# Kernel tuning notes

Measured on AMD Instinct MI355X. Metric: run time of the kernel, lower is better.

The kernel has to match this reference:

```python
import jax, jax.numpy as jnp
import numpy as np

N, M, D = 1024, 32, 512
EPS = 1e-6


def setup_inputs() -> dict:
    key = jax.random.key(0)
    k1, = jax.random.split(key, 1)
    dvecs = jax.random.normal(k1, (N, M, D), dtype=jnp.float32)
    w = jnp.float32(10.0)
    b = jnp.float32(-5.0)
    return {"dvecs": dvecs, "w": w, "b": b}


def reference(dvecs, w, b):
    # dvecs: (N, M, D)
    n, m, d = dvecs.shape
    centroids = dvecs.mean(axis=1)                     # (N, D) full centroids
    # leave-one-out centroid for the reference utterance's own speaker
    c_loo = (dvecs.sum(axis=1, keepdims=True) - dvecs) / (m - 1)   # (N, M, D)

    e_norm = jnp.linalg.norm(dvecs, axis=-1)           # (N, M)
    c_norm = jnp.linalg.norm(centroids, axis=-1)       # (N,)
    c_loo_norm = jnp.linalg.norm(c_loo, axis=-1)       # (N, M)

    # cosine sim against all full centroids: (N, M, N)
    cos = jnp.einsum('jmd,kd->jmk', dvecs, centroids) / (
        e_norm[:, :, None] * c_norm[None, None, :])
    # replace the own-speaker entry with leave-one-out cosine
    loo_cos = jnp.einsum('jmd,jmd->jm', dvecs, c_loo) / (e_norm * c_loo_norm)
    jidx = jnp.arange(n)
    midx = jnp.arange(m)
    cos = cos.at[jidx[:, None], midx[None, :], jidx[:, None]].set(loo_cos)

    # torch.clamp(x, 1e-6) clamps the minimum only
    cos = jnp.maximum(cos, EPS) * w + b

    # softmax embed loss: L[j,i] = -log_softmax(cos[j,i,:])[j]
    logp = jax.nn.log_softmax(cos, axis=-1)
    L = -logp[jidx[:, None], midx[None, :], jidx[:, None]]
    return L.sum()
```

## Files before the change

### kernel.cpp

```cpp
#include <hip/hip_runtime.h>
#include <hip/hip_bf16.h>

#define NSPK 1024
#define MU 32
#define DIM 512
#define DIMP (DIM + 8)
#define NROW (NSPK * MU)
#define EPS 1e-6f

typedef __attribute__((ext_vector_type(4))) float f32x4;
typedef __attribute__((ext_vector_type(2))) long i64x2;

#define GLOAD_LDS16(g, l)                                          \
  __builtin_amdgcn_global_load_lds(                                \
      (const __attribute__((address_space(1))) void*)(g),          \
      (__attribute__((address_space(3))) void*)(l), 16, 0, 0)

__global__ __launch_bounds__(256) void k_prep(
    const float* __restrict__ dvecs,
    char* __restrict__ Af8,
    char* __restrict__ Bf8,
    float* __restrict__ loo)
{
  const int j = blockIdx.x, t = threadIdx.x;
  __shared__ float sD[MU * DIMP];
  __shared__ float sS[DIM];
  __shared__ float sred[4];
  __shared__ float sS2v;
  __shared__ float sInv[MU];

  const float* base = dvecs + (size_t)j * (MU * DIM);

  float s0 = 0.f, s1 = 0.f;
  for (int m = 0; m < MU; ++m) {
    float a = base[m * DIM + t];
    float b = base[m * DIM + t + 256];
    sD[m * DIMP + t] = a;
    sD[m * DIMP + t + 256] = b;
    s0 += a; s1 += b;
  }
  sS[t] = s0; sS[t + 256] = s1;
  __syncthreads();

  float p = s0 * s0 + s1 * s1;
  for (int off = 32; off; off >>= 1) p += __shfl_down(p, off);
  if ((t & 63) == 0) sred[t >> 6] = p;
  __syncthreads();
  if (t == 0) sS2v = sred[0] + sred[1] + sred[2] + sred[3];
  __syncthreads();
  const float S2 = sS2v;

  const int g = t >> 3, l = t & 7;
  float dotS = 0.f, e2 = 0.f;
  for (int i = 0; i < DIM / 8; ++i) {
    int d = i * 8 + l;
    float ev = sD[g * DIMP + d];
    dotS += ev * sS[d];
    e2 += ev * ev;
  }
  for (int off = 4; off; off >>= 1) {
    dotS += __shfl_down(dotS, off);
    e2 += __shfl_down(e2, off);
  }
  if (l == 0) {
    float numer = dotS - e2;
    float d2 = fmaxf(S2 - 2.f * dotS + e2, 1e-30f);
    loo[j * MU + g] = numer / (sqrtf(e2) * sqrtf(d2));
    sInv[g] = 1.f / sqrtf(e2);
  }
  __syncthreads();

  for (int i = 0; i < 8; ++i) {
    int idx = i * 256 + t;
    int m = idx >> 6;
    int c = idx & 63;
    int kt = c >> 2, lk = c & 3;
    float inv = sInv[m];
    const float* src = &sD[m * DIMP + c * 8];
    int b0 = 0, b1 = 0;
    b0 = __builtin_amdgcn_cvt_pk_fp8_f32(src[0] * inv, src[1] * inv, b0, false);
    b0 = __builtin_amdgcn_cvt_pk_fp8_f32(src[2] * inv, src[3] * inv, b0, true);
    b1 = __builtin_amdgcn_cvt_pk_fp8_f32(src[4] * inv, src[5] * inv, b1, false);
    b1 = __builtin_amdgcn_cvt_pk_fp8_f32(src[6] * inv, src[7] * inv, b1, true);
    size_t byte = ((size_t)(j >> 2) << 16) + ((size_t)kt << 12) +
                  ((size_t)(j & 3) << 10) + (lk * 16 + (m & 15)) * 16 +
                  (((m >> 4) & 1) << 3);
    *(int2*)(Af8 + byte) = make_int2(b0, b1);
  }

  if (t < 64) {
    int c = t;
    int kt = c >> 2, lk = c & 3;
    float invc = 1.f / sqrtf(S2);
    const float* src = &sS[c * 8];
    int b0 = 0, b1 = 0;
    b0 = __builtin_amdgcn_cvt_pk_fp8_f32(src[0] * invc, src[1] * invc, b0, false);
    b0 = __builtin_amdgcn_cvt_pk_fp8_f32(src[2] * invc, src[3] * invc, b0, true);
    b1 = __builtin_amdgcn_cvt_pk_fp8_f32(src[4] * invc, src[5] * invc, b1, false);
    b1 = __builtin_amdgcn_cvt_pk_fp8_f32(src[6] * invc, src[7] * invc, b1, true);
    size_t byte = ((size_t)(j >> 7) << 16) + ((size_t)kt << 12) +
                  ((size_t)((j >> 5) & 3) << 10) + (lk * 16 + (j & 15)) * 16 +
                  (((j >> 4) & 1) << 3);
    *(int2*)(Bf8 + byte) = make_int2(b0, b1);
  }
}

__global__ __launch_bounds__(256, 1) void k_gemm(
    const char* __restrict__ Af8,
    const char* __restrict__ Bf8,
    const float* __restrict__ wp,
    float* __restrict__ part,
    float* __restrict__ diag)
{
  __shared__ char ldsA[4 * 4096];
  __shared__ char ldsB[4 * 4096];
  __shared__ float sPart[128][2];

  const int t = threadIdx.x;
  const int w = t >> 6, lane = t & 63;
  const int lr = lane & 15, lk = lane >> 4;
  const int wm = w >> 1, wn = w & 1;
  const int bid = blockIdx.x;
  const int xcd = bid & 7, ii = bid >> 3;
  const int rb = xcd * 32 + (ii >> 3);
  const int cb = ii & 7;

  f32x4 acc[4][4];
#pragma unroll
  for (int a = 0; a < 4; ++a)
#pragma unroll
    for (int b = 0; b < 4; ++b) acc[a][b] = (f32x4)0.f;

  const char* gA = Af8 + ((size_t)rb << 16) + t * 16;
  const char* gB = Bf8 + ((size_t)cb << 16) + t * 16;
  char* dA = &ldsA[t * 16];
  char* dB = &ldsB[t * 16];

#define STAGE(kt, bi)                                     \
  {                                                       \
    GLOAD_LDS16(gA + ((size_t)(kt) << 12), dA + ((bi) << 12)); \
    GLOAD_LDS16(gB + ((size_t)(kt) << 12), dB + ((bi) << 12)); \
  }

  i64x2 aP[2][2], bP[2][2];
  const char* lA0 = &ldsA[(wm * 2) * 1024 + lane * 16];
  const char* lB0 = &ldsB[(wn * 2) * 1024 + lane * 16];

#define DSREAD(set, bi)                                      \
  {                                                          \
    aP[set][0] = *(const i64x2*)(lA0 + ((bi) << 12));        \
    aP[set][1] = *(const i64x2*)(lA0 + ((bi) << 12) + 1024); \
    bP[set][0] = *(const i64x2*)(lB0 + ((bi) << 12));        \
    bP[set][1] = *(const i64x2*)(lB0 + ((bi) << 12) + 1024); \
  }

  STAGE(0, 0);
  STAGE(1, 1);
  STAGE(2, 2);
  asm volatile("s_waitcnt vmcnt(4)" ::: "memory");
  __builtin_amdgcn_s_barrier();
  __builtin_amdgcn_sched_barrier(0);
  DSREAD(0, 0);

#pragma unroll
  for (int kt = 0; kt < 16; ++kt) {
    if (kt <= 13) {
      asm volatile("s_waitcnt vmcnt(2)" ::: "memory");
    } else {
      asm volatile("s_waitcnt vmcnt(0)" ::: "memory");
    }
    __builtin_amdgcn_s_barrier();
    __builtin_amdgcn_sched_barrier(0);

    if (kt <= 12) STAGE(kt + 3, (kt + 3) & 3);
    if (kt < 15) DSREAD((kt + 1) & 1, (kt + 1) & 3);

    if (kt < 15) {
      asm volatile("s_waitcnt lgkmcnt(4)" ::: "memory");
    } else {
      asm volatile("s_waitcnt lgkmcnt(0)" ::: "memory");
    }
    __builtin_amdgcn_sched_barrier(0);

    {
      const int s = kt & 1;
      long av[4] = {aP[s][0].x, aP[s][0].y, aP[s][1].x, aP[s][1].y};
      long bv[4] = {bP[s][0].x, bP[s][0].y, bP[s][1].x, bP[s][1].y};
      __builtin_amdgcn_s_setprio(1);
#pragma unroll
      for (int mf = 0; mf < 4; ++mf)
#pragma unroll
        for (int nf = 0; nf < 4; ++nf)
          acc[mf][nf] = __builtin_amdgcn_mfma_f32_16x16x32_fp8_fp8(
              av[mf], bv[nf], acc[mf][nf], 0, 0, 0);
      __builtin_amdgcn_s_setprio(0);
    }
  }
#undef STAGE
#undef DSREAD

  const float W = *wp;

  if (cb == (rb >> 5)) {
#pragma unroll
    for (int sp = 0; sp < 4; ++sp) {
      const int c = rb * 4 + sp;
      if (wm == (sp >> 1) && wn == ((c >> 6) & 1)) {
        const int nfo = (c >> 4) & 3;
#pragma unroll
        for (int mh = 0; mh < 2; ++mh) {
          f32x4 dsel = acc[(sp & 1) * 2 + mh][0];
#pragma unroll
          for (int nf = 1; nf < 4; ++nf)
            if (nf == nfo) dsel = acc[(sp & 1) * 2 + mh][nf];
          if (lr == (c & 15)) {
#pragma unroll
            for (int i = 0; i < 4; ++i)
              diag[c * 32 + mh * 16 + lk * 4 + i] = dsel[i];
          }
        }
      }
    }
  }

#pragma unroll
  for (int mf = 0; mf < 4; ++mf)
#pragma unroll
    for (int i = 0; i < 4; ++i) {
      float s = 0.f;
#pragma unroll
      for (int nf = 0; nf < 4; ++nf)
        s += __expf((fmaxf(acc[mf][nf][i], EPS) - 1.f) * W);
      s += __shfl_xor(s, 1);
      s += __shfl_xor(s, 2);
      s += __shfl_xor(s, 4);
      s += __shfl_xor(s, 8);
      if (lr == 0) sPart[wm * 64 + mf * 16 + lk * 4 + i][wn] = s;
    }
  __syncthreads();
  if (t < 128)
    part[(size_t)cb * NROW + rb * 128 + t] = sPart[t][0] + sPart[t][1];
}

__global__ __launch_bounds__(256) void k_final1(
    const float* __restrict__ part, const float* __restrict__ loo,
    const float* __restrict__ diag, const float* __restrict__ wp,
    float* __restrict__ p2)
{
  const int t = threadIdx.x;
  const int r = blockIdx.x * 256 + t;
  const float W = *wp;
  float s = 0.f;
#pragma unroll
  for (int c = 0; c < 8; ++c) s += part[(size_t)c * NROW + r];
  const float lt = (fmaxf(loo[r], EPS) - 1.f) * W;
  const float dt = (fmaxf(diag[r], EPS) - 1.f) * W;
  s += __expf(lt) - __expf(dt);
  float v = logf(s) - lt;
  __shared__ float red[4];
  for (int off = 32; off; off >>= 1) v += __shfl_down(v, off);
  if ((t & 63) == 0) red[t >> 6] = v;
  __syncthreads();
  if (t == 0) p2[blockIdx.x] = red[0] + red[1] + red[2] + red[3];
}

__global__ __launch_bounds__(128) void k_final2(
    const float* __restrict__ p2, float* __restrict__ out)
{
  const int t = threadIdx.x;
  float v = p2[t];
  for (int off = 32; off; off >>= 1) v += __shfl_down(v, off);
  __shared__ float red[2];
  if ((t & 63) == 0) red[t >> 6] = v;
  __syncthreads();
  if (t == 0) out[0] = red[0] + red[1];
}

extern "C" void kernel_launch(void* const* d_in, const int* in_sizes, int n_in,
                              void* d_out, int out_size, void* d_ws, size_t ws_size,
                              hipStream_t stream) {
  const float* dvecs = (const float*)d_in[0];
  const float* wptr  = (const float*)d_in[1];
  float* out = (float*)d_out;

  char* ws = (char*)d_ws;
  char* Af8 = ws;            ws += (size_t)NROW * DIM;
  char* Bf8 = ws;            ws += (size_t)NSPK * DIM;
  float* loo  = (float*)ws;  ws += (size_t)NROW * sizeof(float);
  float* diag = (float*)ws;  ws += (size_t)NROW * sizeof(float);
  float* part = (float*)ws;  ws += (size_t)8 * NROW * sizeof(float);
  float* p2   = (float*)ws;

  k_prep<<<NSPK, 256, 0, stream>>>(dvecs, Af8, Bf8, loo);
  k_gemm<<<2048, 256, 0, stream>>>(Af8, Bf8, wptr, part, diag);
  k_final1<<<NROW / 256, 256, 0, stream>>>(part, loo, diag, wptr, p2);
  k_final2<<<1, 128, 0, stream>>>(p2, out);
}
```

Before: 66.19 us.

## Deepen GEMM LDS pipeline to six stages with two k-tiles per barrier; vectorize prep loads

The fp8 GEMM kernel's LDS ring grows from four to six buffers, and the main loop now processes two k-tiles per barrier. It issues two stage loads and two LDS reads per iteration, which halves the number of barriers and deepens the prefetch distance. Separately, the prep kernel loads its input with float4 and splits the member dimension across two thread halves before combining the partial column sums. The changes raise LDS usage and register pressure, and they drop the earlier overlap in which the next tile's LDS reads were issued before the current tile's MFMAs.

```diff
diff --git a/kernel.cpp b/kernel.cpp
--- a/kernel.cpp
+++ b/kernel.cpp
@@ -24,6 +24,7 @@
 {
   const int j = blockIdx.x, t = threadIdx.x;
   __shared__ float sD[MU * DIMP];
+  __shared__ float4 sHalf[2][128];
   __shared__ float sS[DIM];
   __shared__ float sred[4];
   __shared__ float sS2v;
@@ -31,18 +32,28 @@
 
   const float* base = dvecs + (size_t)j * (MU * DIM);
 
-  float s0 = 0.f, s1 = 0.f;
-  for (int m = 0; m < MU; ++m) {
-    float a = base[m * DIM + t];
-    float b = base[m * DIM + t + 256];
-    sD[m * DIMP + t] = a;
-    sD[m * DIMP + t + 256] = b;
-    s0 += a; s1 += b;
-  }
-  sS[t] = s0; sS[t + 256] = s1;
-  __syncthreads();
-
-  float p = s0 * s0 + s1 * s1;
+  const int h = t >> 7, c4 = t & 127;
+  {
+    const float* bp = base + h * 16 * DIM + c4 * 4;
+    float4 cs = make_float4(0.f, 0.f, 0.f, 0.f);
+#pragma unroll
+    for (int m = 0; m < 16; ++m) {
+      float4 v = *(const float4*)(bp + m * DIM);
+      *(float4*)&sD[(h * 16 + m) * DIMP + c4 * 4] = v;
+      cs.x += v.x; cs.y += v.y; cs.z += v.z; cs.w += v.w;
+    }
+    sHalf[h][c4] = cs;
+  }
+  __syncthreads();
+  if (t < 128) {
+    float4 a = sHalf[0][t], b2 = sHalf[1][t];
+    float4 s;
+    s.x = a.x + b2.x; s.y = a.y + b2.y; s.z = a.z + b2.z; s.w = a.w + b2.w;
+    *(float4*)&sS[t * 4] = s;
+  }
+  __syncthreads();
+
+  float p = sS[t] * sS[t] + sS[t + 256] * sS[t + 256];
   for (int off = 32; off; off >>= 1) p += __shfl_down(p, off);
   if ((t & 63) == 0) sred[t >> 6] = p;
   __syncthreads();
@@ -112,8 +123,8 @@
     float* __restrict__ part,
     float* __restrict__ diag)
 {
-  __shared__ char ldsA[4 * 4096];
-  __shared__ char ldsB[4 * 4096];
+  __shared__ char ldsA[6 * 4096];
+  __shared__ char ldsB[6 * 4096];
   __shared__ float sPart[128][2];
 
   const int t = threadIdx.x;
@@ -136,8 +147,8 @@
   char* dA = &ldsA[t * 16];
   char* dB = &ldsB[t * 16];
 
-#define STAGE(kt, bi)                                     \
-  {                                                       \
+#define STAGE(kt, bi)                                          \
+  {                                                            \
     GLOAD_LDS16(gA + ((size_t)(kt) << 12), dA + ((bi) << 12)); \
     GLOAD_LDS16(gB + ((size_t)(kt) << 12), dB + ((bi) << 12)); \
   }
@@ -154,50 +165,54 @@
     bP[set][1] = *(const i64x2*)(lB0 + ((bi) << 12) + 1024); \
   }
 
+#define MFMA_SET(s)                                                      \
+  {                                                                      \
+    long av[4] = {aP[s][0].x, aP[s][0].y, aP[s][1].x, aP[s][1].y};       \
+    long bv[4] = {bP[s][0].x, bP[s][0].y, bP[s][1].x, bP[s][1].y};       \
+    __builtin_amdgcn_s_setprio(1);                                       \
+    _Pragma("unroll")                                                    \
+    for (int mf = 0; mf < 4; ++mf)                                       \
+      _Pragma("unroll")                                                  \
+      for (int nf = 0; nf < 4; ++nf)                                     \
+        acc[mf][nf] = __builtin_amdgcn_mfma_f32_16x16x32_fp8_fp8(        \
+            av[mf], bv[nf], acc[mf][nf], 0, 0, 0);                       \
+    __builtin_amdgcn_s_setprio(0);                                       \
+  }
+
   STAGE(0, 0);
   STAGE(1, 1);
   STAGE(2, 2);
-  asm volatile("s_waitcnt vmcnt(4)" ::: "memory");
-  __builtin_amdgcn_s_barrier();
-  __builtin_amdgcn_sched_barrier(0);
-  DSREAD(0, 0);
-
-#pragma unroll
-  for (int kt = 0; kt < 16; ++kt) {
-    if (kt <= 13) {
-      asm volatile("s_waitcnt vmcnt(2)" ::: "memory");
+  STAGE(3, 3);
+
+#pragma unroll
+  for (int i = 0; i < 8; ++i) {
+    if (i < 7) {
+      asm volatile("s_waitcnt vmcnt(4)" ::: "memory");
     } else {
       asm volatile("s_waitcnt vmcnt(0)" ::: "memory");
     }
     __builtin_amdgcn_s_barrier();
     __builtin_amdgcn_sched_barrier(0);
 
-    if (kt <= 12) STAGE(kt + 3, (kt + 3) & 3);
-    if (kt < 15) DSREAD((kt + 1) & 1, (kt + 1) & 3);
-
-    if (kt < 15) {
-      asm volatile("s_waitcnt lgkmcnt(4)" ::: "memory");
-    } else {
-      asm volatile("s_waitcnt lgkmcnt(0)" ::: "memory");
-    }
+    if (i <= 5) {
+      STAGE(2 * i + 4, (2 * i + 4) % 6);
+      STAGE(2 * i + 5, (2 * i + 5) % 6);
+    }
+
+    DSREAD(0, (2 * i) % 6);
     __builtin_amdgcn_sched_barrier(0);
-
-    {
-      const int s = kt & 1;
-      long av[4] = {aP[s][0].x, aP[s][0].y, aP[s][1].x, aP[s][1].y};
-      long bv[4] = {bP[s][0].x, bP[s][0].y, bP[s][1].x, bP[s][1].y};
-      __builtin_amdgcn_s_setprio(1);
-#pragma unroll
-      for (int mf = 0; mf < 4; ++mf)
-#pragma unroll
-        for (int nf = 0; nf < 4; ++nf)
-          acc[mf][nf] = __builtin_amdgcn_mfma_f32_16x16x32_fp8_fp8(
-              av[mf], bv[nf], acc[mf][nf], 0, 0, 0);
-      __builtin_amdgcn_s_setprio(0);
-    }
+    DSREAD(1, (2 * i + 1) % 6);
+
+    asm volatile("s_waitcnt lgkmcnt(4)" ::: "memory");
+    __builtin_amdgcn_sched_barrier(0);
+    MFMA_SET(0);
+    asm volatile("s_waitcnt lgkmcnt(0)" ::: "memory");
+    __builtin_amdgcn_sched_barrier(0);
+    MFMA_SET(1);
   }
 #undef STAGE
 #undef DSREAD
+#undef MFMA_SET
 
   const float W = *wp;
 
```

New measurement: 61.84 us. -6.6%, faster.
